# Performance work log

Measured on AMD Instinct MI355X. Metric: run time of the kernel, lower is better.

## Reference

```python
import jax, jax.numpy as jnp
import numpy as np
import math
from math import ceil

# --- static configuration (matches init_kwargs / input_specs) ---
T, H, W = 10, 45, 80            # native 720p latent video grid
NUM_WIN = (2, 5, 5)             # num_windows passed to make_720Pwindows_bysize
D_MODEL = 512
HEADS = 4
HEAD_DIM = 128
ROPE_DIMS = (32, 48, 48)        # 3D RoPE split of head_dim over (t, h, w)
THETA = 10000.0
TXT_LEN = 64
N_VID = T * H * W


def _make_windows():
    """Replicates make_720Pwindows_bysize slicing; returns gather/scatter index tables."""
    t, h, w = T, H, W
    rnt, rnh, rnw = NUM_WIN
    scale = math.sqrt(45 * 80 / (h * w))
    rh, rw = round(h * scale), round(w * scale)
    wh, ww = ceil(rh / rnh), ceil(rw / rnw)
    wt = ceil(min(t, 30) / rnt)
    nt, nh, nw = ceil(t / wt), ceil(h / wh), ceil(w / ww)
    lin = np.arange(t * h * w).reshape(t, h, w)
    wins = []
    for iw in range(nw):
        for ih in range(nh):
            for it in range(nt):
                ts = slice(it * wt, min((it + 1) * wt, t))
                hs = slice(ih * wh, min((ih + 1) * wh, h))
                ws = slice(iw * ww, min((iw + 1) * ww, w))
                blk = lin[ts, hs, ws].reshape(-1)
                if blk.size:
                    wins.append(blk)
    assert len({x.size for x in wins}) == 1, 'chosen dims give uniform windows'
    idx = np.stack(wins)                      # [n_win, win_size] gather index
    src = np.argsort(idx.reshape(-1))         # inverse permutation (un-window)
    return idx, src

WIN_IDX_NP, SRC_IDX_NP = _make_windows()
N_WIN, WIN_SIZE = WIN_IDX_NP.shape


def _rope_tables():
    """3D RoPE cos/sin per vid token: head_dim split over (t,h,w) axes, interleaved pairs."""
    tt = np.broadcast_to(np.arange(T)[:, None, None], (T, H, W)).reshape(-1)
    hh = np.broadcast_to(np.arange(H)[None, :, None], (T, H, W)).reshape(-1)
    ww = np.broadcast_to(np.arange(W)[None, None, :], (T, H, W)).reshape(-1)
    cos_l, sin_l = [], []
    for pos, d in zip((tt, hh, ww), ROPE_DIMS):
        inv = 1.0 / (THETA ** (np.arange(0, d, 2, dtype=np.float64) / d))
        ang = pos[:, None].astype(np.float64) * inv[None, :]
        ang = np.repeat(ang, 2, axis=-1)
        cos_l.append(np.cos(ang))
        sin_l.append(np.sin(ang))
    cos = np.concatenate(cos_l, -1).astype(np.float32)
    sin = np.concatenate(sin_l, -1).astype(np.float32)
    return jnp.asarray(cos), jnp.asarray(sin)  # each [N_VID, HEAD_DIM]

ROPE_COS, ROPE_SIN = _rope_tables()


def _rotate_half(x):
    # '... (d r) -> ... d r' with r=2, then (-x2, x1) re-interleaved
    xr = x.reshape(x.shape[:-1] + (-1, 2))
    x1, x2 = xr[..., 0], xr[..., 1]
    return jnp.stack((-x2, x1), axis=-1).reshape(x.shape)


def _apply_rope(x, cos, sin):
    # x: [N, heads, D]; cos/sin: [N, D]
    return x * cos[:, None, :] + _rotate_half(x) * sin[:, None, :]


def setup_inputs() -> dict:
    key = jax.random.key(0)
    ks = jax.random.split(key, 6)
    s = 1.0 / math.sqrt(D_MODEL)
    return {
        'vid': jax.random.normal(ks[0], (N_VID, D_MODEL), jnp.float32),
        'txt': jax.random.normal(ks[1], (TXT_LEN, D_MODEL), jnp.float32),
        'w_qkv_vid': jax.random.normal(ks[2], (D_MODEL, 3 * D_MODEL), jnp.float32) * s,
        'w_qkv_txt': jax.random.normal(ks[3], (D_MODEL, 3 * D_MODEL), jnp.float32) * s,
        'w_out_vid': jax.random.normal(ks[4], (D_MODEL, D_MODEL), jnp.float32) * s,
        'w_out_txt': jax.random.normal(ks[5], (D_MODEL, D_MODEL), jnp.float32) * s,
    }


def reference(vid, txt, w_qkv_vid, w_qkv_txt, w_out_vid, w_out_txt):
    win_idx = jnp.asarray(WIN_IDX_NP)
    src_idx = jnp.asarray(SRC_IDX_NP)
    # per-modality QKV projection (MMModule: separate vid/txt weights)
    qkv_v = (vid @ w_qkv_vid).reshape(N_VID, 3, HEADS, HEAD_DIM)
    qv, kv, vv = qkv_v[:, 0], qkv_v[:, 1], qkv_v[:, 2]
    qv = _apply_rope(qv, ROPE_COS, ROPE_SIN)   # 3D RoPE on video q/k only
    kv = _apply_rope(kv, ROPE_COS, ROPE_SIN)
    qkv_t = (txt @ w_qkv_txt).reshape(TXT_LEN, 3, HEADS, HEAD_DIM)
    qt, kt, vt = qkv_t[:, 0], qkv_t[:, 1], qkv_t[:, 2]

    def win_cat(xv, xt):
        xw = xv[win_idx]
        xtb = jnp.broadcast_to(xt[None], (N_WIN,) + xt.shape)    # txt repeated per window
        return jnp.concatenate([xw, xtb], axis=1)                # [n_win, S, H, D]

    q, k, v = win_cat(qv, qt), win_cat(kv, kt), win_cat(vv, vt)
    scale = 1.0 / math.sqrt(HEAD_DIM)
    scores = jnp.einsum('wqhd,wkhd->whqk', q, k) * scale         # [n_win, H, S, S]
    probs = jax.nn.softmax(scores, axis=-1)
    out = jnp.einsum('whqk,wkhd->wqhd', probs, v)                # [n_win, S, H, D]
    # un-window vid tokens (inverse permutation), mean-coalesce txt over windows
    out_v = out[:, :WIN_SIZE].reshape(N_WIN * WIN_SIZE, D_MODEL)[src_idx]
    out_t = out[:, WIN_SIZE:].mean(axis=0).reshape(TXT_LEN, D_MODEL)
    return jnp.concatenate([out_v @ w_out_vid, out_t @ w_out_txt], axis=0)
```

## Files before the change

### kernel.cpp

```cpp
#include <hip/hip_runtime.h>
#include <hip/hip_bf16.h>


typedef unsigned short u16;
typedef unsigned int   u32;
typedef float v4f __attribute__((ext_vector_type(4)));
typedef short v8s __attribute__((ext_vector_type(8)));

#define N_VID    36000
#define MPAD     36096
#define DM       512
#define NW       50
#define WSZ      720
#define SEQ      784
#define SP       832
#define QK_SCALE 0.08838834764831845f
#define L2THETA  13.287712379549449f

union U8 { uint4 u; u16 s[8]; };

__device__ __forceinline__ u16 f2b(float f) {
  u32 u = __builtin_bit_cast(u32, f);
  u32 r = (u + 0x7FFFu + ((u >> 16) & 1u)) >> 16;
  return (u16)r;
}
__device__ __forceinline__ float b2f(u16 h) {
  u32 u = ((u32)h) << 16;
  return __builtin_bit_cast(float, u);
}
__device__ __forceinline__ u32 pkhi(float lo, float hi) {
  return __builtin_amdgcn_perm(__builtin_bit_cast(u32, hi),
                               __builtin_bit_cast(u32, lo), 0x07060302u);
}
__device__ __forceinline__ int vperm4(int l0) {
  return (l0 & ~31) + (((l0 & 15) >> 2) << 3) + (((l0 >> 4) & 1) << 2);
}

__device__ __forceinline__ void gload_lds16(const void* g, void* l) {
  __builtin_amdgcn_global_load_lds(
      (const __attribute__((address_space(1))) void*)g,
      (__attribute__((address_space(3))) void*)l,
      16, 0, 0);
}

__global__ __launch_bounds__(256) void k_prep(const float* __restrict__ vid,
                                              const float* __restrict__ txt,
                                              u16* __restrict__ vid_b,
                                              u16* __restrict__ txt_b,
                                              const float* __restrict__ wqv,
                                              const float* __restrict__ wqt,
                                              const float* __restrict__ wov,
                                              u16* __restrict__ o0,
                                              u16* __restrict__ o1,
                                              u16* __restrict__ o2) {
  __shared__ u16 lt[64 * 72];
  int t = threadIdx.x;
  if (blockIdx.x < 9056) {
    int id  = blockIdx.x * 256 + t;
    int row = id >> 6, oct = id & 63;
    U8 o;
    if (row < MPAD) {
      if (row < N_VID) {
        const float* s = vid + (size_t)row * DM + oct * 8;
        float4 a = *(const float4*)s, b = *(const float4*)(s + 4);
        o.s[0]=f2b(a.x); o.s[1]=f2b(a.y); o.s[2]=f2b(a.z); o.s[3]=f2b(a.w);
        o.s[4]=f2b(b.x); o.s[5]=f2b(b.y); o.s[6]=f2b(b.z); o.s[7]=f2b(b.w);
      } else { o.u = make_uint4(0,0,0,0); }
      *(uint4*)&vid_b[(size_t)row * DM + oct * 8] = o.u;
    } else {
      int tr = row - MPAD;
      if (tr >= 128) return;
      if (tr < 64) {
        const float* s = txt + (size_t)tr * DM + oct * 8;
        float4 a = *(const float4*)s, b = *(const float4*)(s + 4);
        o.s[0]=f2b(a.x); o.s[1]=f2b(a.y); o.s[2]=f2b(a.z); o.s[3]=f2b(a.w);
        o.s[4]=f2b(b.x); o.s[5]=f2b(b.y); o.s[6]=f2b(b.z); o.s[7]=f2b(b.w);
      } else { o.u = make_uint4(0,0,0,0); }
      *(uint4*)&txt_b[(size_t)tr * DM + oct * 8] = o.u;
    }
    return;
  }
  int b = blockIdx.x - 9056;
  const float* src; u16* dst; int N; int tb;
  if (b < 192)      { src = wqv; dst = o0; N = 1536; tb = b; }
  else if (b < 384) { src = wqt; dst = o1; N = 1536; tb = b - 192; }
  else              { src = wov; dst = o2; N = 512;  tb = b - 384; }
  int kt = tb & 7, nt = tb >> 3;
  int k0 = kt * 64, n0 = nt * 64;
#pragma unroll
  for (int pass = 0; pass < 16; ++pass) {
    int kl = pass * 4 + (t >> 6), nl = t & 63;
    float v = src[(size_t)(k0 + kl) * N + n0 + nl];
    lt[nl * 72 + kl] = f2b(v);
  }
  __syncthreads();
#pragma unroll
  for (int pass = 0; pass < 2; ++pass) {
    int slot = pass * 256 + t;
    int nr = slot >> 3, ko = slot & 7;
    U8 o;
#pragma unroll
    for (int j = 0; j < 8; ++j) o.s[j] = lt[nr * 72 + ko * 8 + j];
    *(uint4*)&dst[(size_t)(n0 + nr) * 512 + k0 + ko * 8] = o.u;
  }
}

template <int F32OUT>
__device__ __forceinline__ void gemm_body(const u16* __restrict__ A,
                                          const u16* __restrict__ Bt,
                                          void* __restrict__ Cout,
                                          int N, int K, int Mstore,
                                          int m0, int n0) {
  __shared__ u16 lA[128 * 32];
  __shared__ u16 lB[128 * 32];
  int t = threadIdx.x, wv = t >> 6, L = t & 63;
  int wm = wv & 1, wn = wv >> 1;
  v4f acc[4][4] = {};
  const int kiters = K >> 5;
  const u16* ga = A + (size_t)(m0 + wv * 32 + (L >> 2)) * K + (L & 3) * 8;
  const u16* gb = Bt + (size_t)(n0 + wv * 32 + (L >> 2)) * K + (L & 3) * 8;
  u16* la = lA + (wv * 32) * 32;
  u16* lb = lB + (wv * 32) * 32;
  for (int kt = 0; kt < kiters; ++kt) {
    __syncthreads();
    gload_lds16(ga,                 la);
    gload_lds16(ga + (size_t)16 * K, la + 16 * 32);
    gload_lds16(gb,                 lb);
    gload_lds16(gb + (size_t)16 * K, lb + 16 * 32);
    ga += 32; gb += 32;
    __syncthreads();
    v8s af[4], bf[4];
#pragma unroll
    for (int i = 0; i < 4; ++i) {
      af[i] = *(const v8s*)&lA[(wm * 64 + i * 16 + (L & 15)) * 32 + (L >> 4) * 8];
      bf[i] = *(const v8s*)&lB[(wn * 64 + i * 16 + (L & 15)) * 32 + (L >> 4) * 8];
    }
#pragma unroll
    for (int i = 0; i < 4; ++i)
#pragma unroll
      for (int j = 0; j < 4; ++j)
        acc[i][j] = __builtin_amdgcn_mfma_f32_16x16x32_bf16(af[i], bf[j], acc[i][j], 0, 0, 0);
  }
#pragma unroll
  for (int i = 0; i < 4; ++i) {
#pragma unroll
    for (int r = 0; r < 4; ++r) {
      int row = m0 + wm * 64 + i * 16 + (L >> 4) * 4 + r;
      if (row < Mstore) {
#pragma unroll
        for (int j = 0; j < 4; ++j) {
          int col = n0 + wn * 64 + j * 16 + (L & 15);
          if (F32OUT) ((float*)Cout)[(size_t)row * N + col] = acc[i][j][r];
          else        ((u16*)Cout)[(size_t)row * N + col] = f2b(acc[i][j][r]);
        }
      }
    }
  }
}

__global__ __launch_bounds__(256) void k_gemm_qkv(const u16* __restrict__ vid_b,
                                                  const u16* __restrict__ wt_qv,
                                                  u16* __restrict__ qkv_v,
                                                  const u16* __restrict__ txt_b,
                                                  const u16* __restrict__ wt_qt,
                                                  u16* __restrict__ qkv_t) {
  if (blockIdx.y < 12) {
    gemm_body<0>(vid_b, wt_qv, qkv_v, 1536, 512, MPAD, blockIdx.x * 128, blockIdx.y * 128);
  } else {
    if (blockIdx.x >= 12) return;
    gemm_body<0>(txt_b, wt_qt, qkv_t, 1536, 512, 128, 0, blockIdx.x * 128);
  }
}

__global__ __launch_bounds__(256) void k_ropegather(const u16* __restrict__ qkv,
                                                    const u16* __restrict__ qkvt,
                                                    u16* __restrict__ Q,
                                                    u16* __restrict__ K,
                                                    u16* __restrict__ Vt) {
  __shared__ u16 lv[512 * 18];
  int t = threadIdx.x;
  int w = blockIdx.y;
  if (blockIdx.x >= 45) {
    int tb = (blockIdx.x - 45) * 256 + t;
#pragma unroll
    for (int k = 0; k < 4; ++k) {
      int o = tb * 4 + k;
      int h = o >> 10, p64 = (o >> 4) & 63, c8 = o & 15;
      U8 q, kk;
      q.u  = *(const uint4*)&qkvt[(size_t)p64 * 1536 + h * 128 + c8 * 8];
      kk.u = *(const uint4*)&qkvt[(size_t)p64 * 1536 + 512 + h * 128 + c8 * 8];
#pragma unroll
      for (int j = 0; j < 8; ++j) q.s[j] = f2b(b2f(q.s[j]) * QK_SCALE);
      size_t base = (((size_t)w * 4 + h) * SP + WSZ + p64) * 128 + c8 * 8;
      *(uint4*)&Q[base] = q.u;
      *(uint4*)&K[base] = kk.u;
    }
#pragma unroll
    for (int k = 0; k < 8; ++k) {
      int vr = tb * 8 + k;
      int h = vr >> 11, ch = (vr >> 4) & 127, run = vr & 15;
      int l0 = WSZ + run * 4;
      uint2 o;
      u16* os = (u16*)&o;
#pragma unroll
      for (int j = 0; j < 4; ++j)
        os[j] = qkvt[(size_t)(l0 - WSZ + j) * 1536 + 1024 + h * 128 + ch];
      *(uint2*)&Vt[(((size_t)w * 4 + h) * 128 + ch) * SP + vperm4(l0)] = o;
    }
    return;
  }
  int pt = blockIdx.x;
  int p_local = t >> 4;
  int p = pt * 16 + p_local;
  int iw = w / 10; int r10 = w - iw * 10; int ih = r10 >> 1; int it = r10 & 1;
  int dt = p / 144; int rem = p - dt * 144; int dh = rem >> 4; int dw = rem & 15;
  int tt = it * 5 + dt, hh = ih * 9 + dh, wx = iw * 16 + dw;
  int n = tt * 3600 + hh * 80 + wx;
  const size_t qrow = (size_t)n * 1536;
#pragma unroll
  for (int it2 = 0; it2 < 12; ++it2) {
    int oct = it2 * 16 + (t & 15);
    int col = oct * 8;
    U8 x; x.u = *(const uint4*)&qkv[qrow + col];
    if (col < 1024) {
      int cc = col & 511; int h = cc >> 7; int ch = cc & 127;
      int pos, i0; float dinv;
      if (ch < 32)      { pos = tt; i0 = ch >> 1;        dinv = 1.f / 32.f; }
      else if (ch < 80) { pos = hh; i0 = (ch - 32) >> 1; dinv = 1.f / 48.f; }
      else              { pos = wx; i0 = (ch - 80) >> 1; dinv = 1.f / 48.f; }
      bool isQ = col < 512;
      float sc = isQ ? QK_SCALE : 1.0f;
      U8 o;
#pragma unroll
      for (int pr = 0; pr < 4; ++pr) {
        float inv = exp2f(-2.f * (float)(i0 + pr) * dinv * L2THETA);
        float ang = (float)pos * inv;
        float s, c; __sincosf(ang, &s, &c);
        float x0 = b2f(x.s[2 * pr]), x1 = b2f(x.s[2 * pr + 1]);
        o.s[2 * pr]     = f2b((x0 * c - x1 * s) * sc);
        o.s[2 * pr + 1] = f2b((x1 * c + x0 * s) * sc);
      }
      u16* dst = isQ ? Q : K;
      *(uint4*)&dst[(((size_t)w * 4 + h) * SP + p) * 128 + ch] = o.u;
    } else {
      int cv = col - 1024;
#pragma unroll
      for (int j = 0; j < 8; ++j) lv[(cv + j) * 18 + p_local] = x.s[j];
    }
  }
  __syncthreads();
#pragma unroll
  for (int it3 = 0; it3 < 4; ++it3) {
    int slot = it3 * 256 + t; int cv = slot >> 1; int half = slot & 1;
    U8 o;
#pragma unroll
    for (int j = 0; j < 8; ++j) o.s[j] = lv[cv * 18 + half * 8 + j];
    int h = cv >> 7, ch = cv & 127;
    int P0 = pt * 16 + half * 8;
    size_t base = (((size_t)w * 4 + h) * 128 + ch) * SP;
    *(uint2*)&Vt[base + vperm4(P0)]     = make_uint2(o.u.x, o.u.y);
    *(uint2*)&Vt[base + vperm4(P0 + 4)] = make_uint2(o.u.z, o.u.w);
  }
}

__global__ __launch_bounds__(256) void k_attn(const u16* __restrict__ Q,
                                              const u16* __restrict__ Kb,
                                              const u16* __restrict__ Vt,
                                              u16* __restrict__ outr,
                                              float* __restrict__ txt_acc) {
  __shared__ u16 lK[4 * 64 * 32];
  __shared__ u16 lV[2 * 128 * 32];
  int t = threadIdx.x, wv = t >> 6, L = t & 63;
  int id = blockIdx.x;
  int xcd = id & 7, sidx = id >> 3;
  int whg = sidx / 7;  int qt = sidx - whg * 7;
  int wh = whg * 8 + xcd;
  int w = wh >> 2, h = wh & 3;
  size_t whq = ((size_t)wh) * SP * 128;
  int q0 = qt * 128 + wv * 32;
  if (q0 > 800) q0 = 800;
  int colL = L & 15, quad = L >> 4;
  v8s qf[2][4];
#pragma unroll
  for (int s = 0; s < 2; ++s) {
    const u16* qp = Q + whq + (size_t)(q0 + s * 16 + colL) * 128 + quad * 8;
#pragma unroll
    for (int kc = 0; kc < 4; ++kc) qf[s][kc] = *(const v8s*)(qp + kc * 32);
  }
  float li[2] = {0.f, 0.f};
  v4f O[2][8] = {};

  for (int kt = 0; kt < 13; ++kt) {
    __syncthreads();
#pragma unroll
    for (int pass = 0; pass < 4; ++pass) {
      int cr = wv * 64 + pass * 16 + (L >> 2);
      int kc = cr >> 6, row = cr & 63;
      gload_lds16(Kb + whq + (size_t)(kt * 64 + row) * 128 + kc * 32 + (L & 3) * 8,
                  (u16*)lK + (size_t)(wv * 64 + pass * 16) * 32);
      int kc2 = cr >> 7, ch = cr & 127;
      gload_lds16(Vt + whq + (size_t)ch * SP + kt * 64 + kc2 * 32 + (L & 3) * 8,
                  (u16*)lV + (size_t)(wv * 64 + pass * 16) * 32);
    }
    __syncthreads();

    v4f ST[2][4] = {};
#pragma unroll
    for (int kc = 0; kc < 4; ++kc) {
#pragma unroll
      for (int nbk = 0; nbk < 4; ++nbk) {
        v8s kf = *(const v8s*)&lK[(kc * 64 + nbk * 16 + colL) * 32 + quad * 8];
        ST[0][nbk] = __builtin_amdgcn_mfma_f32_16x16x32_bf16(kf, qf[0][kc], ST[0][nbk], 0, 0, 0);
        ST[1][nbk] = __builtin_amdgcn_mfma_f32_16x16x32_bf16(kf, qf[1][kc], ST[1][nbk], 0, 0, 0);
      }
    }

    union { v8s v; u32 wd[4]; } Bf[2][2];
#pragma unroll
    for (int s = 0; s < 2; ++s) {
#pragma unroll
      for (int nbk = 0; nbk < 4; ++nbk) {
        float ev[4];
        if (kt * 64 + nbk * 16 < SEQ) {
#pragma unroll
          for (int r = 0; r < 4; ++r) {
            float e = __expf(ST[s][nbk][r]);
            u32 tb = __builtin_bit_cast(u32, e) & 0xFFFF0000u;
            float tf = __builtin_bit_cast(float, tb);
            li[s] += tf;
            ev[r] = tf;
          }
        } else {
#pragma unroll
          for (int r = 0; r < 4; ++r) ev[r] = 0.f;
        }
        Bf[nbk >> 1][s].wd[(nbk & 1) * 2 + 0] = pkhi(ev[0], ev[1]);
        Bf[nbk >> 1][s].wd[(nbk & 1) * 2 + 1] = pkhi(ev[2], ev[3]);
      }
    }

#pragma unroll
    for (int kc2 = 0; kc2 < 2; ++kc2) {
#pragma unroll
      for (int nbo = 0; nbo < 8; ++nbo) {
        v8s af = *(const v8s*)&lV[(kc2 * 128 + nbo * 16 + colL) * 32 + quad * 8];
        O[0][nbo] = __builtin_amdgcn_mfma_f32_16x16x32_bf16(af, Bf[kc2][0].v, O[0][nbo], 0, 0, 0);
        O[1][nbo] = __builtin_amdgcn_mfma_f32_16x16x32_bf16(af, Bf[kc2][1].v, O[1][nbo], 0, 0, 0);
      }
    }
  }

  float linv[2];
#pragma unroll
  for (int s = 0; s < 2; ++s) {
    float v = li[s];
    v += __shfl_xor(v, 16);
    v += __shfl_xor(v, 32);
    linv[s] = 1.f / v;
  }

  int iw = w / 10; int r10 = w - iw * 10; int ih = r10 >> 1; int it = r10 & 1;
#pragma unroll
  for (int s = 0; s < 2; ++s) {
    int p = q0 + s * 16 + colL;
    if (p < WSZ) {
      int dt = p / 144; int rem = p - dt * 144; int dh = rem >> 4; int dw = rem & 15;
      int n = (it * 5 + dt) * 3600 + (ih * 9 + dh) * 80 + iw * 16 + dw;
      size_t rowbase = (size_t)n * DM + h * 128 + quad * 4;
#pragma unroll
      for (int nbo = 0; nbo < 8; ++nbo) {
        uint2 st;
        st.x = (u32)f2b(O[s][nbo][0] * linv[s]) | ((u32)f2b(O[s][nbo][1] * linv[s]) << 16);
        st.y = (u32)f2b(O[s][nbo][2] * linv[s]) | ((u32)f2b(O[s][nbo][3] * linv[s]) << 16);
        *(uint2*)&outr[rowbase + nbo * 16] = st;
      }
    } else if (p < SEQ) {
      size_t rb = (size_t)(p - WSZ) * DM + h * 128 + quad * 4;
#pragma unroll
      for (int nbo = 0; nbo < 8; ++nbo)
#pragma unroll
        for (int r = 0; r < 4; ++r)
          atomicAdd(&txt_acc[rb + nbo * 16 + r], O[s][nbo][r] * linv[s] * 0.02f);
    }
  }
}

__global__ __launch_bounds__(256) void k_gemm_out(const u16* __restrict__ A,
                                                  const u16* __restrict__ Bt,
                                                  float* __restrict__ out,
                                                  const float* __restrict__ acc,
                                                  const float* __restrict__ wo) {
  if (blockIdx.x < 282) {
    gemm_body<1>(A, Bt, out, 512, 512, N_VID, blockIdx.x * 128, blockIdx.y * 128);
    return;
  }
  int r = (blockIdx.x - 282) * 4 + blockIdx.y;
  int t = threadIdx.x;
  float s0 = 0.f, s1 = 0.f;
  for (int k = 0; k < 512; ++k) {
    float a = acc[r * 512 + k];
    s0 = fmaf(a, wo[k * 512 + t], s0);
    s1 = fmaf(a, wo[k * 512 + t + 256], s1);
  }
  float* ob = out + (size_t)N_VID * DM;
  ob[(size_t)r * 512 + t] = s0;
  ob[(size_t)r * 512 + t + 256] = s1;
}

extern "C" void kernel_launch(void* const* d_in, const int* in_sizes, int n_in,
                              void* d_out, int out_size, void* d_ws, size_t ws_size,
                              hipStream_t stream) {
  const float* vid       = (const float*)d_in[0];
  const float* txt       = (const float*)d_in[1];
  const float* w_qkv_vid = (const float*)d_in[2];
  const float* w_qkv_txt = (const float*)d_in[3];
  const float* w_out_vid = (const float*)d_in[4];
  const float* w_out_txt = (const float*)d_in[5];
  float* out = (float*)d_out;
  char* ws = (char*)d_ws;

  size_t off = 0;
  u16* vid_b   = (u16*)(ws + off); off += (size_t)MPAD * DM * 2;
  u16* txt_b   = (u16*)(ws + off); off += 128 * DM * 2;
  u16* wt_qv   = (u16*)(ws + off); off += 1536 * 512 * 2;
  u16* wt_qt   = (u16*)(ws + off); off += 1536 * 512 * 2;
  u16* wt_ov   = (u16*)(ws + off); off += 512 * 512 * 2;
  u16* qkv_v   = (u16*)(ws + off); off += (size_t)MPAD * 1536 * 2;
  u16* qkv_t   = (u16*)(ws + off); off += 128 * 1536 * 2;
  u16* Qb      = (u16*)(ws + off); off += (size_t)NW * 4 * SP * 128 * 2;
  u16* Kb      = (u16*)(ws + off); off += (size_t)NW * 4 * SP * 128 * 2;
  u16* Vtb     = (u16*)(ws + off); off += (size_t)NW * 4 * 128 * SP * 2;
  float* tacc  = (float*)(ws + off); off += 64 * 512 * 4;
  u16* out_rows = vid_b;

  hipMemsetAsync(tacc, 0, 64 * 512 * 4, stream);

  k_prep<<<9504, 256, 0, stream>>>(vid, txt, vid_b, txt_b,
                                   w_qkv_vid, w_qkv_txt, w_out_vid,
                                   wt_qv, wt_qt, wt_ov);

  k_gemm_qkv<<<dim3(282, 13), 256, 0, stream>>>(vid_b, wt_qv, qkv_v,
                                                txt_b, wt_qt, qkv_t);

  k_ropegather<<<dim3(49, 50), 256, 0, stream>>>(qkv_v, qkv_t, Qb, Kb, Vtb);

  k_attn<<<1400, 256, 0, stream>>>(Qb, Kb, Vtb, out_rows, tacc);

  k_gemm_out<<<dim3(298, 4), 256, 0, stream>>>(out_rows, wt_ov, out, tacc, w_out_txt);
}
```

Baseline: 475.4 us.

## Double-buffer K/V LDS tiles, fold log2e into Q scale, skip dead waves

```diff
diff --git a/kernel.cpp b/kernel.cpp
--- a/kernel.cpp
+++ b/kernel.cpp
@@ -14,7 +14,7 @@
 #define WSZ      720
 #define SEQ      784
 #define SP       832
-#define QK_SCALE 0.08838834764831845f
+#define QK_SCALE_L2E 0.12751743f
 #define L2THETA  13.287712379549449f
 
 union U8 { uint4 u; u16 s[8]; };
@@ -190,7 +190,7 @@
       q.u  = *(const uint4*)&qkvt[(size_t)p64 * 1536 + h * 128 + c8 * 8];
       kk.u = *(const uint4*)&qkvt[(size_t)p64 * 1536 + 512 + h * 128 + c8 * 8];
 #pragma unroll
-      for (int j = 0; j < 8; ++j) q.s[j] = f2b(b2f(q.s[j]) * QK_SCALE);
+      for (int j = 0; j < 8; ++j) q.s[j] = f2b(b2f(q.s[j]) * QK_SCALE_L2E);
       size_t base = (((size_t)w * 4 + h) * SP + WSZ + p64) * 128 + c8 * 8;
       *(uint4*)&Q[base] = q.u;
       *(uint4*)&K[base] = kk.u;
@@ -229,7 +229,7 @@
       else if (ch < 80) { pos = hh; i0 = (ch - 32) >> 1; dinv = 1.f / 48.f; }
       else              { pos = wx; i0 = (ch - 80) >> 1; dinv = 1.f / 48.f; }
       bool isQ = col < 512;
-      float sc = isQ ? QK_SCALE : 1.0f;
+      float sc = isQ ? QK_SCALE_L2E : 1.0f;
       U8 o;
 #pragma unroll
       for (int pr = 0; pr < 4; ++pr) {
@@ -268,8 +268,8 @@
                                               const u16* __restrict__ Vt,
                                               u16* __restrict__ outr,
                                               float* __restrict__ txt_acc) {
-  __shared__ u16 lK[4 * 64 * 32];
-  __shared__ u16 lV[2 * 128 * 32];
+  __shared__ u16 lK[2][4 * 64 * 32];
+  __shared__ u16 lV[2][2 * 128 * 32];
   int t = threadIdx.x, wv = t >> 6, L = t & 63;
   int id = blockIdx.x;
   int xcd = id & 7, sidx = id >> 3;
@@ -278,6 +278,7 @@
   int w = wh >> 2, h = wh & 3;
   size_t whq = ((size_t)wh) * SP * 128;
   int q0 = qt * 128 + wv * 32;
+  bool live = q0 < SEQ;
   if (q0 > 800) q0 = 800;
   int colL = L & 15, quad = L >> 4;
   v8s qf[2][4];
@@ -290,65 +291,84 @@
   float li[2] = {0.f, 0.f};
   v4f O[2][8] = {};
 
-  for (int kt = 0; kt < 13; ++kt) {
-    __syncthreads();
+  auto stage = [&](int kt, int buf) {
 #pragma unroll
     for (int pass = 0; pass < 4; ++pass) {
       int cr = wv * 64 + pass * 16 + (L >> 2);
       int kc = cr >> 6, row = cr & 63;
       gload_lds16(Kb + whq + (size_t)(kt * 64 + row) * 128 + kc * 32 + (L & 3) * 8,
-                  (u16*)lK + (size_t)(wv * 64 + pass * 16) * 32);
+                  (u16*)&lK[buf][0] + (size_t)(wv * 64 + pass * 16) * 32);
       int kc2 = cr >> 7, ch = cr & 127;
       gload_lds16(Vt + whq + (size_t)ch * SP + kt * 64 + kc2 * 32 + (L & 3) * 8,
-                  (u16*)lV + (size_t)(wv * 64 + pass * 16) * 32);
-    }
+                  (u16*)&lV[buf][0] + (size_t)(wv * 64 + pass * 16) * 32);
+    }
+  };
+
+  stage(0, 0);
+  __syncthreads();
+
+  for (int kt = 0; kt < 13; ++kt) {
+    int cur = kt & 1;
+    if (kt < 12) stage(kt + 1, cur ^ 1);
+
+    if (live) {
+      const u16* lKc = &lK[cur][0];
+      const u16* lVc = &lV[cur][0];
+
+      v4f ST[2][4] = {};
+      __builtin_amdgcn_s_setprio(1);
+#pragma unroll
+      for (int kc = 0; kc < 4; ++kc) {
+#pragma unroll
+        for (int nbk = 0; nbk < 4; ++nbk) {
+          v8s kf = *(const v8s*)&lKc[(kc * 64 + nbk * 16 + colL) * 32 + quad * 8];
+          ST[0][nbk] = __builtin_amdgcn_mfma_f32_16x16x32_bf16(kf, qf[0][kc], ST[0][nbk], 0, 0, 0);
+          ST[1][nbk] = __builtin_amdgcn_mfma_f32_16x16x32_bf16(kf, qf[1][kc], ST[1][nbk], 0, 0, 0);
+        }
+      }
+      __builtin_amdgcn_s_setprio(0);
+
+      union { v8s v; u32 wd[4]; } Bf[2][2];
+#pragma unroll
+      for (int s = 0; s < 2; ++s) {
+#pragma unroll
+        for (int nbk = 0; nbk < 4; ++nbk) {
+          float ev[4];
+          if (kt * 64 + nbk * 16 < SEQ) {
+#pragma unroll
+            for (int r = 0; r < 4; ++r) {
+              float e = __builtin_amdgcn_exp2f(ST[s][nbk][r]);
+              u32 tb = __builtin_bit_cast(u32, e) & 0xFFFF0000u;
+              float tf = __builtin_bit_cast(float, tb);
+              li[s] += tf;
+              ev[r] = tf;
+            }
+          } else {
+#pragma unroll
+            for (int r = 0; r < 4; ++r) ev[r] = 0.f;
+          }
+          Bf[nbk >> 1][s].wd[(nbk & 1) * 2 + 0] = pkhi(ev[0], ev[1]);
+          Bf[nbk >> 1][s].wd[(nbk & 1) * 2 + 1] = pkhi(ev[2], ev[3]);
+        }
+      }
+
+      __builtin_amdgcn_s_setprio(1);
+#pragma unroll
+      for (int kc2 = 0; kc2 < 2; ++kc2) {
+#pragma unroll
+        for (int nbo = 0; nbo < 8; ++nbo) {
+          v8s af = *(const v8s*)&lVc[(kc2 * 128 + nbo * 16 + colL) * 32 + quad * 8];
+          O[0][nbo] = __builtin_amdgcn_mfma_f32_16x16x32_bf16(af, Bf[kc2][0].v, O[0][nbo], 0, 0, 0);
+          O[1][nbo] = __builtin_amdgcn_mfma_f32_16x16x32_bf16(af, Bf[kc2][1].v, O[1][nbo], 0, 0, 0);
+        }
+      }
+      __builtin_amdgcn_s_setprio(0);
+    }
+
     __syncthreads();
-
-    v4f ST[2][4] = {};
-#pragma unroll
-    for (int kc = 0; kc < 4; ++kc) {
-#pragma unroll
-      for (int nbk = 0; nbk < 4; ++nbk) {
-        v8s kf = *(const v8s*)&lK[(kc * 64 + nbk * 16 + colL) * 32 + quad * 8];
-        ST[0][nbk] = __builtin_amdgcn_mfma_f32_16x16x32_bf16(kf, qf[0][kc], ST[0][nbk], 0, 0, 0);
-        ST[1][nbk] = __builtin_amdgcn_mfma_f32_16x16x32_bf16(kf, qf[1][kc], ST[1][nbk], 0, 0, 0);
-      }
-    }
-
-    union { v8s v; u32 wd[4]; } Bf[2][2];
-#pragma unroll
-    for (int s = 0; s < 2; ++s) {
-#pragma unroll
-      for (int nbk = 0; nbk < 4; ++nbk) {
-        float ev[4];
-        if (kt * 64 + nbk * 16 < SEQ) {
-#pragma unroll
-          for (int r = 0; r < 4; ++r) {
-            float e = __expf(ST[s][nbk][r]);
-            u32 tb = __builtin_bit_cast(u32, e) & 0xFFFF0000u;
-            float tf = __builtin_bit_cast(float, tb);
-            li[s] += tf;
-            ev[r] = tf;
-          }
-        } else {
-#pragma unroll
-          for (int r = 0; r < 4; ++r) ev[r] = 0.f;
-        }
-        Bf[nbk >> 1][s].wd[(nbk & 1) * 2 + 0] = pkhi(ev[0], ev[1]);
-        Bf[nbk >> 1][s].wd[(nbk & 1) * 2 + 1] = pkhi(ev[2], ev[3]);
-      }
-    }
-
-#pragma unroll
-    for (int kc2 = 0; kc2 < 2; ++kc2) {
-#pragma unroll
-      for (int nbo = 0; nbo < 8; ++nbo) {
-        v8s af = *(const v8s*)&lV[(kc2 * 128 + nbo * 16 + colL) * 32 + quad * 8];
-        O[0][nbo] = __builtin_amdgcn_mfma_f32_16x16x32_bf16(af, Bf[kc2][0].v, O[0][nbo], 0, 0, 0);
-        O[1][nbo] = __builtin_amdgcn_mfma_f32_16x16x32_bf16(af, Bf[kc2][1].v, O[1][nbo], 0, 0, 0);
-      }
-    }
-  }
+  }
+
+  if (!live) return;
 
   float linv[2];
 #pragma unroll
```

After: 462.4 us. -2.7%, faster.
